# Optimization experiments

Measured on AMD Instinct MI355X. Metric: run time of the kernel, lower is better.

Reference implementation:

```python
import jax, jax.numpy as jnp
import numpy as np

DIM = 1024
HEADS = 16
DIM_HEAD = 64


def setup_inputs() -> dict:
    key = jax.random.key(0)
    k1, k2 = jax.random.split(key)
    x = jax.random.normal(k1, (2, 2048, DIM), dtype=jnp.float32)
    # to_qkv: Linear(dim, 3*heads*dim_head, bias=False); torch weight is [out,in],
    # we store the transposed [in,out] form for x @ W.
    W_qkv = jax.random.normal(k2, (DIM, 3 * HEADS * DIM_HEAD), dtype=jnp.float32) * (DIM ** -0.5)
    return {"x": x, "W_qkv": W_qkv}


def reference(x, W_qkv):
    b, n, _ = x.shape
    h, d = HEADS, DIM_HEAD
    scale = d ** -0.5
    qkv = x @ W_qkv                              # [b, n, 3*h*d]
    q, k, v = jnp.split(qkv, 3, axis=-1)
    # 'b n (h d) -> b h n d'
    q = q.reshape(b, n, h, d).transpose(0, 2, 1, 3)
    k = k.reshape(b, n, h, d).transpose(0, 2, 1, 3)
    v = v.reshape(b, n, h, d).transpose(0, 2, 1, 3)
    dots = jnp.einsum('bhnd,bhmd->bhnm', q, k) * scale
    attn = jax.nn.softmax(dots, axis=-1)
    out = jnp.einsum('bhnm,bhmd->bhnd', attn, v)
    out = out.transpose(0, 2, 1, 3).reshape(b, n, h * d)  # 'b h n d -> b n (h d)'
    return out + x  # residual (to_out is never applied in the source forward)
```

## Files before the change

kernel.cpp:

```cpp
#include <hip/hip_runtime.h>

#define DIM   1024
#define NQKV  3072
#define SEQ   2048
#define HEADS 16
#define DHEAD 64
#define M_TOT 4096

typedef __bf16 bf16;
typedef __bf16 bf16x8 __attribute__((ext_vector_type(8)));
typedef float  f32x4  __attribute__((ext_vector_type(4)));

typedef const __attribute__((address_space(1))) unsigned int gu32;
typedef __attribute__((address_space(3))) unsigned int su32;

static __device__ __forceinline__ unsigned short f2b(float f) {
    bf16 h = (bf16)f;
    return __builtin_bit_cast(unsigned short, h);
}

#define CAST_BLOCKS (M_TOT * DIM / (256 * 4))
#define TR_NB (NQKV / 64)
__global__ void prep_kernel(const float* __restrict__ x,
                            unsigned short* __restrict__ xb,
                            const float* __restrict__ W,
                            unsigned short* __restrict__ Wt) {
    __shared__ float tile[64][65];
    const int id  = blockIdx.x;
    const int tid = threadIdx.x;
    if (id < CAST_BLOCKS) {
        int i = (id * 256 + tid) * 4;
        float4 v = *(const float4*)(x + i);
        ushort4 o;
        o.x = f2b(v.x); o.y = f2b(v.y); o.z = f2b(v.z); o.w = f2b(v.w);
        *(ushort4*)(xb + i) = o;
    } else {
        int t  = id - CAST_BLOCKS;
        int nb = t % TR_NB;
        int kb = t / TR_NB;
        #pragma unroll
        for (int p = 0; p < 4; p++) {
            int kl = p * 16 + (tid >> 4);
            int nl = (tid & 15) * 4;
            float4 v = *(const float4*)&W[(size_t)(kb * 64 + kl) * NQKV + nb * 64 + nl];
            tile[nl + 0][kl] = v.x;
            tile[nl + 1][kl] = v.y;
            tile[nl + 2][kl] = v.z;
            tile[nl + 3][kl] = v.w;
        }
        __syncthreads();
        #pragma unroll
        for (int p = 0; p < 2; p++) {
            int nl = p * 32 + (tid >> 3);
            int k8 = (tid & 7) * 8;
            int n  = nb * 64 + nl;
            float s = (n < 1024) ? 0.18033688f : 1.0f;
            float4 a = *(const float4*)&tile[nl][k8];
            float4 b = *(const float4*)&tile[nl][k8 + 4];
            ushort4 o0, o1;
            o0.x = f2b(a.x * s); o0.y = f2b(a.y * s); o0.z = f2b(a.z * s); o0.w = f2b(a.w * s);
            o1.x = f2b(b.x * s); o1.y = f2b(b.y * s); o1.z = f2b(b.z * s); o1.w = f2b(b.w * s);
            uint4 pk;
            pk.x = ((unsigned)o0.y << 16) | o0.x;
            pk.y = ((unsigned)o0.w << 16) | o0.z;
            pk.z = ((unsigned)o1.y << 16) | o1.x;
            pk.w = ((unsigned)o1.w << 16) | o1.z;
            *(uint4*)&Wt[(size_t)n * DIM + kb * 64 + k8] = pk;
        }
    }
}

#define LDC 136
__global__ __launch_bounds__(256) void qkv_gemm_kernel(
    const unsigned short* __restrict__ A,
    const unsigned short* __restrict__ Bt,
    unsigned short* __restrict__ Qw,
    unsigned short* __restrict__ Kw,
    unsigned short* __restrict__ Vtw)
{
    __shared__ __align__(16) unsigned char smem[65536];
    unsigned short* Cs = (unsigned short*)smem;

    const int tid  = threadIdx.x;
    const int m0   = blockIdx.y * 128;
    const int n0   = blockIdx.x * 128;
    const int w    = tid >> 6;
    const int lane = tid & 63;
    const int l16  = lane & 15;
    const int quad = lane >> 4;
    const int wm   = (w >> 1) * 64;
    const int wn   = (w & 1) * 64;
    const int srow = lane >> 3;
    const int scol = ((lane & 7) ^ srow) * 8;
    const int xa   = l16 & 7;

    f32x4 acc[4][4];
    const f32x4 fzero = {0.f, 0.f, 0.f, 0.f};
    for (int i = 0; i < 4; i++)
        for (int j = 0; j < 4; j++) acc[i][j] = fzero;

    const unsigned short* Ag = A  + (size_t)(m0 + w * 32 + srow) * DIM + scol;
    const unsigned short* Bg = Bt + (size_t)(n0 + w * 32 + srow) * DIM + scol;

    {
        unsigned short* As0 = (unsigned short*)smem;
        unsigned short* Bs0 = (unsigned short*)(smem + 16384);
        #pragma unroll
        for (int j = 0; j < 4; j++) {
            __builtin_amdgcn_global_load_lds((gu32*)(Ag + (size_t)j * 8 * DIM),
                                             (su32*)&As0[(w * 32 + j * 8) * 64], 16, 0, 0);
            __builtin_amdgcn_global_load_lds((gu32*)(Bg + (size_t)j * 8 * DIM),
                                             (su32*)&Bs0[(w * 32 + j * 8) * 64], 16, 0, 0);
        }
    }
    __syncthreads();

    for (int ki = 0; ki < 16; ki++) {
        const int cur = ki & 1, nxt = cur ^ 1;
        if (ki < 15) {
            const int kt = (ki + 1) * 64;
            unsigned short* Asn = (unsigned short*)(smem + nxt * 32768);
            unsigned short* Bsn = (unsigned short*)(smem + nxt * 32768 + 16384);
            #pragma unroll
            for (int j = 0; j < 4; j++) {
                __builtin_amdgcn_global_load_lds((gu32*)(Ag + kt + (size_t)j * 8 * DIM),
                                                 (su32*)&Asn[(w * 32 + j * 8) * 64], 16, 0, 0);
                __builtin_amdgcn_global_load_lds((gu32*)(Bg + kt + (size_t)j * 8 * DIM),
                                                 (su32*)&Bsn[(w * 32 + j * 8) * 64], 16, 0, 0);
            }
        }
        const unsigned short* As = (const unsigned short*)(smem + cur * 32768);
        const unsigned short* Bs = (const unsigned short*)(smem + cur * 32768 + 16384);
        #pragma unroll
        for (int s = 0; s < 2; s++) {
            const int col = ((s * 4 + quad) ^ xa) * 8;
            bf16x8 af[4], bfr[4];
            #pragma unroll
            for (int i = 0; i < 4; i++) {
                af[i]  = *(const bf16x8*)(&As[(wm + i * 16 + l16) * 64 + col]);
                bfr[i] = *(const bf16x8*)(&Bs[(wn + i * 16 + l16) * 64 + col]);
            }
            #pragma unroll
            for (int i = 0; i < 4; i++)
                #pragma unroll
                for (int j = 0; j < 4; j++)
                    acc[i][j] = __builtin_amdgcn_mfma_f32_16x16x32_bf16(af[i], bfr[j], acc[i][j], 0, 0, 0);
        }
        __syncthreads();
    }

    const int part = n0 >> 10;
    const int h0   = (n0 & 1023) >> 6;
    const int b    = m0 >> 11;
    const int np0  = m0 & 2047;

    if (part < 2) {
        #pragma unroll
        for (int i = 0; i < 4; i++)
            #pragma unroll
            for (int j = 0; j < 4; j++)
                #pragma unroll
                for (int r = 0; r < 4; r++)
                    Cs[(wm + i * 16 + quad * 4 + r) * LDC + wn + j * 16 + l16] = f2b(acc[i][j][r]);
        __syncthreads();
        unsigned short* dst = (part == 0) ? Qw : Kw;
        #pragma unroll
        for (int pass = 0; pass < 8; pass++) {
            int mi = pass * 16 + (tid >> 4);
            int ci = (tid & 15) * 8;
            uint4 v = *(const uint4*)&Cs[mi * LDC + ci];
            int bh = b * HEADS + h0 + (ci >> 6);
            *(uint4*)&dst[((size_t)bh * SEQ + np0 + mi) * DHEAD + (ci & 63)] = v;
        }
    } else {
        #pragma unroll
        for (int i = 0; i < 4; i++)
            #pragma unroll
            for (int j = 0; j < 4; j++) {
                ushort4 pk;
                pk.x = f2b(acc[i][j][0]); pk.y = f2b(acc[i][j][1]);
                pk.z = f2b(acc[i][j][2]); pk.w = f2b(acc[i][j][3]);
                *(ushort4*)&Cs[(wn + j * 16 + l16) * LDC + wm + i * 16 + quad * 4] = pk;
            }
        __syncthreads();
        #pragma unroll
        for (int pass = 0; pass < 8; pass++) {
            int ci = pass * 16 + (tid >> 4);
            int mi = (tid & 15) * 8;
            uint4 v = *(const uint4*)&Cs[ci * LDC + mi];
            int bh = b * HEADS + h0 + (ci >> 6);
            *(uint4*)&Vtw[((size_t)bh * DHEAD + (ci & 63)) * SEQ + np0 + mi] = v;
        }
    }
}

#define KT 16
__global__ __launch_bounds__(512, 4) void attn_kernel(
    const unsigned short* __restrict__ Qw,
    const unsigned short* __restrict__ Kw,
    const unsigned short* __restrict__ Vtw,
    const float* __restrict__ x,
    float* __restrict__ out)
{
    __shared__ __align__(16) unsigned char smem[65536];
    unsigned short* base = (unsigned short*)smem;
    float* scratch = (float*)smem;

    const int id  = blockIdx.x;
    const int qt  = id >> 5;
    const int bh  = ((id & 7) << 2) | ((id >> 3) & 3);
    const int tid = threadIdx.x;
    const int w   = tid >> 6, lane = tid & 63;
    const int l16 = lane & 15, quad = lane >> 4;
    const int g   = w & 3;
    const int p   = w >> 2;
    const int xq  = l16 & 7;

    const unsigned short* Qb = Qw + ((size_t)bh * SEQ + qt * 128 + g * 32 + l16) * DHEAD;
    bf16x8 qf[2][2];
    #pragma unroll
    for (int qh = 0; qh < 2; qh++) {
        qf[qh][0] = *(const bf16x8*)(Qb + qh * 16 * DHEAD + quad * 8);
        qf[qh][1] = *(const bf16x8*)(Qb + qh * 16 * DHEAD + 32 + quad * 8);
    }

    bf16x8 ones;
    #pragma unroll
    for (int j = 0; j < 8; j++) ones[j] = (bf16)1.0f;

    f32x4 o[2][4], dsum[2];
    const f32x4 fzero = {0.f, 0.f, 0.f, 0.f};
    #pragma unroll
    for (int qh = 0; qh < 2; qh++) {
        #pragma unroll
        for (int d = 0; d < 4; d++) o[qh][d] = fzero;
        dsum[qh] = fzero;
    }

    const unsigned short* Kg = Kw  + (size_t)bh * SEQ * DHEAD;
    const unsigned short* Vg = Vtw + (size_t)bh * DHEAD * SEQ;

    const int sl   = lane >> 3;
    const int c16s = (lane & 7) ^ sl;
    const int pr   = 8 * w + sl;
    const int rlog = ((pr >> 2) & 3) * 8 + ((pr >> 4) & 1) * 4 + (pr & 3) + (pr & 32);
    const size_t koff = (size_t)rlog * DHEAD + c16s * 8;
    const size_t voff = (size_t)pr * SEQ + c16s * 8;

    {
        unsigned short* Kd = base + w * 512;
        unsigned short* Vd = base + 8192 + w * 512;
        __builtin_amdgcn_global_load_lds((gu32*)(Kg + koff),                         (su32*)Kd, 16, 0, 0);
        __builtin_amdgcn_global_load_lds((gu32*)(Kg + (size_t)1024 * DHEAD + koff), (su32*)(Kd + 4096), 16, 0, 0);
        __builtin_amdgcn_global_load_lds((gu32*)(Vg + voff),                         (su32*)Vd, 16, 0, 0);
        __builtin_amdgcn_global_load_lds((gu32*)(Vg + voff + 1024),                  (su32*)(Vd + 4096), 16, 0, 0);
    }
    __syncthreads();

    for (int t = 0; t < KT; t++) {
        const int cur = t & 1, nxt = cur ^ 1;
        if (t + 1 < KT) {
            const size_t kb = (size_t)((t + 1) * 64) * DHEAD;
            const int kv = (t + 1) * 64;
            unsigned short* Kd = base + nxt * 16384 + w * 512;
            unsigned short* Vd = base + nxt * 16384 + 8192 + w * 512;
            __builtin_amdgcn_global_load_lds((gu32*)(Kg + kb + koff),                         (su32*)Kd, 16, 0, 0);
            __builtin_amdgcn_global_load_lds((gu32*)(Kg + kb + (size_t)1024 * DHEAD + koff), (su32*)(Kd + 4096), 16, 0, 0);
            __builtin_amdgcn_global_load_lds((gu32*)(Vg + voff + kv),                        (su32*)Vd, 16, 0, 0);
            __builtin_amdgcn_global_load_lds((gu32*)(Vg + voff + 1024 + kv),                 (su32*)(Vd + 4096), 16, 0, 0);
        }

        const unsigned short* Kb = base + cur * 16384 + p * 4096;
        const unsigned short* Vb = base + cur * 16384 + 8192 + p * 4096;

        f32x4 sacc[2][4];
        #pragma unroll
        for (int qh = 0; qh < 2; qh++)
            #pragma unroll
            for (int ki = 0; ki < 4; ki++) sacc[qh][ki] = fzero;
        #pragma unroll
        for (int s = 0; s < 2; s++) {
            const int col = ((s * 4 + quad) ^ xq) * 8;
            #pragma unroll
            for (int ki = 0; ki < 4; ki++) {
                bf16x8 kf = *(const bf16x8*)(&Kb[(ki * 16 + l16) * 64 + col]);
                sacc[0][ki] = __builtin_amdgcn_mfma_f32_16x16x32_bf16(kf, qf[0][s], sacc[0][ki], 0, 0, 0);
                sacc[1][ki] = __builtin_amdgcn_mfma_f32_16x16x32_bf16(kf, qf[1][s], sacc[1][ki], 0, 0, 0);
            }
        }

        bf16x8 pf[2][2];
        #pragma unroll
        for (int qh = 0; qh < 2; qh++)
            #pragma unroll
            for (int s = 0; s < 2; s++)
                #pragma unroll
                for (int half = 0; half < 2; half++) {
                    int ki = 2 * s + half;
                    #pragma unroll
                    for (int r = 0; r < 4; r++)
                        pf[qh][s][half * 4 + r] = (bf16)__builtin_amdgcn_exp2f(sacc[qh][ki][r]);
                }

        #pragma unroll
        for (int s = 0; s < 2; s++) {
            const int col = ((s * 4 + quad) ^ xq) * 8;
            dsum[0] = __builtin_amdgcn_mfma_f32_16x16x32_bf16(pf[0][s], ones, dsum[0], 0, 0, 0);
            dsum[1] = __builtin_amdgcn_mfma_f32_16x16x32_bf16(pf[1][s], ones, dsum[1], 0, 0, 0);
            #pragma unroll
            for (int d = 0; d < 4; d++) {
                bf16x8 vf = *(const bf16x8*)(&Vb[(d * 16 + l16) * 64 + col]);
                o[0][d] = __builtin_amdgcn_mfma_f32_16x16x32_bf16(pf[0][s], vf, o[0][d], 0, 0, 0);
                o[1][d] = __builtin_amdgcn_mfma_f32_16x16x32_bf16(pf[1][s], vf, o[1][d], 0, 0, 0);
            }
        }
        __syncthreads();
    }

    #pragma unroll
    for (int ch = 0; ch < 2; ch++) {
        if (ch) __syncthreads();
        if (p == 1) {
            float* sc = scratch + ((size_t)(g * 64 + lane)) * 20;
            #pragma unroll
            for (int di = 0; di < 4; di++)
                *(f32x4*)(sc + di * 4) = o[ch][di];
            *(f32x4*)(sc + 16) = dsum[ch];
        }
        __syncthreads();
        if (p == 0) {
            float* sc = scratch + ((size_t)(g * 64 + lane)) * 20;
            #pragma unroll
            for (int di = 0; di < 4; di++)
                o[ch][di] += *(const f32x4*)(sc + di * 4);
            dsum[ch] += *(const f32x4*)(sc + 16);
        }
    }

    if (p == 0) {
        const int b = bh >> 4, h = bh & 15;
        #pragma unroll
        for (int ch = 0; ch < 2; ch++) {
            float lr[4];
            #pragma unroll
            for (int r = 0; r < 4; r++) lr[r] = __builtin_amdgcn_rcpf(dsum[ch][r]);
            #pragma unroll
            for (int di = 0; di < 4; di++)
                #pragma unroll
                for (int r = 0; r < 4; r++) {
                    int np  = qt * 128 + g * 32 + ch * 16 + quad * 4 + r;
                    int col = h * 64 + di * 16 + l16;
                    size_t gidx = ((size_t)(b * SEQ + np)) * DIM + col;
                    out[gidx] = o[ch][di][r] * lr[r] + x[gidx];
                }
        }
    }
}

extern "C" void kernel_launch(void* const* d_in, const int* in_sizes, int n_in,
                              void* d_out, int out_size, void* d_ws, size_t ws_size,
                              hipStream_t stream) {
    const float* x  = (const float*)d_in[0];
    const float* Wq = (const float*)d_in[1];
    float* out = (float*)d_out;

    unsigned short* xb = (unsigned short*)d_ws;
    unsigned short* Wt = xb + (size_t)M_TOT * DIM;
    unsigned short* Qw = Wt + (size_t)NQKV * DIM;
    unsigned short* Kw = Qw + (size_t)32 * SEQ * DHEAD;
    unsigned short* Vt = Kw + (size_t)32 * SEQ * DHEAD;

    prep_kernel<<<CAST_BLOCKS + TR_NB * (DIM / 64), 256, 0, stream>>>(x, xb, Wq, Wt);
    qkv_gemm_kernel<<<dim3(NQKV / 128, M_TOT / 128), 256, 0, stream>>>(xb, Wt, Qw, Kw, Vt);
    attn_kernel<<<(SEQ / 128) * 32, 512, 0, stream>>>(Qw, Kw, Vt, x, out);
}
```

Before: 147.3 us.

## Double attention query tile per block and halve per-iteration KV tile

Each attention block now covers 256 queries instead of 128, with each wave group handling 64 query rows (four 16-row MFMA fragments). Each iteration now streams 64 keys and splits them across the two wave halves, so the loop runs 32 times instead of 16. The aim is to double the reuse of every K/V fragment loaded into LDS across query rows and to halve total K/V global traffic. In exchange the grid shrinks to 256 blocks, and more accumulator registers are needed, so launch bounds drop to 2 blocks per CU. That may cut occupancy and latency hiding.

```diff
diff --git a/kernel.cpp b/kernel.cpp
--- a/kernel.cpp
+++ b/kernel.cpp
@@ -194,8 +194,7 @@
     }
 }
 
-#define KT 16
-__global__ __launch_bounds__(512, 4) void attn_kernel(
+__global__ __launch_bounds__(512, 2) void attn_kernel(
     const unsigned short* __restrict__ Qw,
     const unsigned short* __restrict__ Kw,
     const unsigned short* __restrict__ Vtw,
@@ -216,10 +215,10 @@
     const int p   = w >> 2;
     const int xq  = l16 & 7;
 
-    const unsigned short* Qb = Qw + ((size_t)bh * SEQ + qt * 128 + g * 32 + l16) * DHEAD;
-    bf16x8 qf[2][2];
+    const unsigned short* Qb = Qw + ((size_t)bh * SEQ + qt * 256 + g * 64 + l16) * DHEAD;
+    bf16x8 qf[4][2];
     #pragma unroll
-    for (int qh = 0; qh < 2; qh++) {
+    for (int qh = 0; qh < 4; qh++) {
         qf[qh][0] = *(const bf16x8*)(Qb + qh * 16 * DHEAD + quad * 8);
         qf[qh][1] = *(const bf16x8*)(Qb + qh * 16 * DHEAD + 32 + quad * 8);
     }
@@ -228,10 +227,10 @@
     #pragma unroll
     for (int j = 0; j < 8; j++) ones[j] = (bf16)1.0f;
 
-    f32x4 o[2][4], dsum[2];
+    f32x4 o[4][4], dsum[4];
     const f32x4 fzero = {0.f, 0.f, 0.f, 0.f};
     #pragma unroll
-    for (int qh = 0; qh < 2; qh++) {
+    for (int qh = 0; qh < 4; qh++) {
         #pragma unroll
         for (int d = 0; d < 4; d++) o[qh][d] = fzero;
         dsum[qh] = fzero;
@@ -247,72 +246,60 @@
     const size_t koff = (size_t)rlog * DHEAD + c16s * 8;
     const size_t voff = (size_t)pr * SEQ + c16s * 8;
 
-    {
-        unsigned short* Kd = base + w * 512;
-        unsigned short* Vd = base + 8192 + w * 512;
-        __builtin_amdgcn_global_load_lds((gu32*)(Kg + koff),                         (su32*)Kd, 16, 0, 0);
-        __builtin_amdgcn_global_load_lds((gu32*)(Kg + (size_t)1024 * DHEAD + koff), (su32*)(Kd + 4096), 16, 0, 0);
-        __builtin_amdgcn_global_load_lds((gu32*)(Vg + voff),                         (su32*)Vd, 16, 0, 0);
-        __builtin_amdgcn_global_load_lds((gu32*)(Vg + voff + 1024),                  (su32*)(Vd + 4096), 16, 0, 0);
-    }
+    __builtin_amdgcn_global_load_lds((gu32*)(Kg + koff), (su32*)(base + w * 512), 16, 0, 0);
+    __builtin_amdgcn_global_load_lds((gu32*)(Vg + voff), (su32*)(base + 4096 + w * 512), 16, 0, 0);
     __syncthreads();
 
-    for (int t = 0; t < KT; t++) {
+    for (int t = 0; t < 32; t++) {
         const int cur = t & 1, nxt = cur ^ 1;
-        if (t + 1 < KT) {
+        if (t + 1 < 32) {
             const size_t kb = (size_t)((t + 1) * 64) * DHEAD;
             const int kv = (t + 1) * 64;
-            unsigned short* Kd = base + nxt * 16384 + w * 512;
-            unsigned short* Vd = base + nxt * 16384 + 8192 + w * 512;
-            __builtin_amdgcn_global_load_lds((gu32*)(Kg + kb + koff),                         (su32*)Kd, 16, 0, 0);
-            __builtin_amdgcn_global_load_lds((gu32*)(Kg + kb + (size_t)1024 * DHEAD + koff), (su32*)(Kd + 4096), 16, 0, 0);
-            __builtin_amdgcn_global_load_lds((gu32*)(Vg + voff + kv),                        (su32*)Vd, 16, 0, 0);
-            __builtin_amdgcn_global_load_lds((gu32*)(Vg + voff + 1024 + kv),                 (su32*)(Vd + 4096), 16, 0, 0);
-        }
-
-        const unsigned short* Kb = base + cur * 16384 + p * 4096;
-        const unsigned short* Vb = base + cur * 16384 + 8192 + p * 4096;
-
-        f32x4 sacc[2][4];
-        #pragma unroll
-        for (int qh = 0; qh < 2; qh++)
-            #pragma unroll
-            for (int ki = 0; ki < 4; ki++) sacc[qh][ki] = fzero;
+            __builtin_amdgcn_global_load_lds((gu32*)(Kg + kb + koff),
+                                             (su32*)(base + nxt * 8192 + w * 512), 16, 0, 0);
+            __builtin_amdgcn_global_load_lds((gu32*)(Vg + voff + kv),
+                                             (su32*)(base + nxt * 8192 + 4096 + w * 512), 16, 0, 0);
+        }
+
+        const unsigned short* Kb = base + cur * 8192;
+        const unsigned short* Vb = base + cur * 8192 + 4096;
+
+        f32x4 sacc[4][2];
+        #pragma unroll
+        for (int qh = 0; qh < 4; qh++)
+            #pragma unroll
+            for (int ki = 0; ki < 2; ki++) sacc[qh][ki] = fzero;
         #pragma unroll
         for (int s = 0; s < 2; s++) {
             const int col = ((s * 4 + quad) ^ xq) * 8;
             #pragma unroll
-            for (int ki = 0; ki < 4; ki++) {
-                bf16x8 kf = *(const bf16x8*)(&Kb[(ki * 16 + l16) * 64 + col]);
-                sacc[0][ki] = __builtin_amdgcn_mfma_f32_16x16x32_bf16(kf, qf[0][s], sacc[0][ki], 0, 0, 0);
-                sacc[1][ki] = __builtin_amdgcn_mfma_f32_16x16x32_bf16(kf, qf[1][s], sacc[1][ki], 0, 0, 0);
-            }
-        }
-
-        bf16x8 pf[2][2];
-        #pragma unroll
-        for (int qh = 0; qh < 2; qh++)
-            #pragma unroll
-            for (int s = 0; s < 2; s++)
-                #pragma unroll
-                for (int half = 0; half < 2; half++) {
-                    int ki = 2 * s + half;
-                    #pragma unroll
-                    for (int r = 0; r < 4; r++)
-                        pf[qh][s][half * 4 + r] = (bf16)__builtin_amdgcn_exp2f(sacc[qh][ki][r]);
-                }
-
-        #pragma unroll
-        for (int s = 0; s < 2; s++) {
-            const int col = ((s * 4 + quad) ^ xq) * 8;
-            dsum[0] = __builtin_amdgcn_mfma_f32_16x16x32_bf16(pf[0][s], ones, dsum[0], 0, 0, 0);
-            dsum[1] = __builtin_amdgcn_mfma_f32_16x16x32_bf16(pf[1][s], ones, dsum[1], 0, 0, 0);
-            #pragma unroll
-            for (int d = 0; d < 4; d++) {
-                bf16x8 vf = *(const bf16x8*)(&Vb[(d * 16 + l16) * 64 + col]);
-                o[0][d] = __builtin_amdgcn_mfma_f32_16x16x32_bf16(pf[0][s], vf, o[0][d], 0, 0, 0);
-                o[1][d] = __builtin_amdgcn_mfma_f32_16x16x32_bf16(pf[1][s], vf, o[1][d], 0, 0, 0);
-            }
+            for (int ki = 0; ki < 2; ki++) {
+                bf16x8 kf = *(const bf16x8*)(&Kb[(p * 32 + ki * 16 + l16) * 64 + col]);
+                #pragma unroll
+                for (int qh = 0; qh < 4; qh++)
+                    sacc[qh][ki] = __builtin_amdgcn_mfma_f32_16x16x32_bf16(kf, qf[qh][s], sacc[qh][ki], 0, 0, 0);
+            }
+        }
+
+        bf16x8 pf[4];
+        #pragma unroll
+        for (int qh = 0; qh < 4; qh++)
+            #pragma unroll
+            for (int ki = 0; ki < 2; ki++)
+                #pragma unroll
+                for (int r = 0; r < 4; r++)
+                    pf[qh][ki * 4 + r] = (bf16)__builtin_amdgcn_exp2f(sacc[qh][ki][r]);
+
+        const int colv = ((p * 4 + quad) ^ xq) * 8;
+        #pragma unroll
+        for (int qh = 0; qh < 4; qh++)
+            dsum[qh] = __builtin_amdgcn_mfma_f32_16x16x32_bf16(pf[qh], ones, dsum[qh], 0, 0, 0);
+        #pragma unroll
+        for (int d = 0; d < 4; d++) {
+            bf16x8 vf = *(const bf16x8*)(&Vb[(d * 16 + l16) * 64 + colv]);
+            #pragma unroll
+            for (int qh = 0; qh < 4; qh++)
+                o[qh][d] = __builtin_amdgcn_mfma_f32_16x16x32_bf16(pf[qh], vf, o[qh][d], 0, 0, 0);
         }
         __syncthreads();
     }
@@ -321,37 +308,45 @@
     for (int ch = 0; ch < 2; ch++) {
         if (ch) __syncthreads();
         if (p == 1) {
-            float* sc = scratch + ((size_t)(g * 64 + lane)) * 20;
-            #pragma unroll
-            for (int di = 0; di < 4; di++)
-                *(f32x4*)(sc + di * 4) = o[ch][di];
-            *(f32x4*)(sc + 16) = dsum[ch];
+            float* sc = scratch + ((size_t)(g * 64 + lane)) * 40;
+            #pragma unroll
+            for (int q2 = 0; q2 < 2; q2++) {
+                int qh = ch * 2 + q2;
+                #pragma unroll
+                for (int di = 0; di < 4; di++)
+                    *(f32x4*)(sc + q2 * 20 + di * 4) = o[qh][di];
+                *(f32x4*)(sc + q2 * 20 + 16) = dsum[qh];
+            }
         }
         __syncthreads();
         if (p == 0) {
-            float* sc = scratch + ((size_t)(g * 64 + lane)) * 20;
-            #pragma unroll
-            for (int di = 0; di < 4; di++)
-                o[ch][di] += *(const f32x4*)(sc + di * 4);
-            dsum[ch] += *(const f32x4*)(sc + 16);
+            float* sc = scratch + ((size_t)(g * 64 + lane)) * 40;
+            #pragma unroll
+            for (int q2 = 0; q2 < 2; q2++) {
+                int qh = ch * 2 + q2;
+                #pragma unroll
+                for (int di = 0; di < 4; di++)
+                    o[qh][di] += *(const f32x4*)(sc + q2 * 20 + di * 4);
+                dsum[qh] += *(const f32x4*)(sc + q2 * 20 + 16);
+            }
         }
     }
 
     if (p == 0) {
         const int b = bh >> 4, h = bh & 15;
         #pragma unroll
-        for (int ch = 0; ch < 2; ch++) {
+        for (int qh = 0; qh < 4; qh++) {
             float lr[4];
             #pragma unroll
-            for (int r = 0; r < 4; r++) lr[r] = __builtin_amdgcn_rcpf(dsum[ch][r]);
+            for (int r = 0; r < 4; r++) lr[r] = __builtin_amdgcn_rcpf(dsum[qh][r]);
             #pragma unroll
             for (int di = 0; di < 4; di++)
                 #pragma unroll
                 for (int r = 0; r < 4; r++) {
-                    int np  = qt * 128 + g * 32 + ch * 16 + quad * 4 + r;
+                    int np  = qt * 256 + g * 64 + qh * 16 + quad * 4 + r;
                     int col = h * 64 + di * 16 + l16;
                     size_t gidx = ((size_t)(b * SEQ + np)) * DIM + col;
-                    out[gidx] = o[ch][di][r] * lr[r] + x[gidx];
+                    out[gidx] = o[qh][di][r] * lr[r] + x[gidx];
                 }
         }
     }
@@ -372,5 +367,5 @@
 
     prep_kernel<<<CAST_BLOCKS + TR_NB * (DIM / 64), 256, 0, stream>>>(x, xb, Wq, Wt);
     qkv_gemm_kernel<<<dim3(NQKV / 128, M_TOT / 128), 256, 0, stream>>>(xb, Wt, Qw, Kw, Vt);
-    attn_kernel<<<(SEQ / 128) * 32, 512, 0, stream>>>(Qw, Kw, Vt, x, out);
-}
+    attn_kernel<<<(SEQ / 256) * 32, 512, 0, stream>>>(Qw, Kw, Vt, x, out);
+}
```

New measurement: 149.6 us. About the same (+1.5%).
